# Performance work log

Hardware: AMD Instinct MI355X
Metric: run time of the kernel (lower is better)

Reference implementation:

```python
import jax, jax.numpy as jnp
import numpy as np

B, S, E, H = 2, 2048, 768, 12
DK = E // H


def setup_inputs() -> dict:
    key = jax.random.key(0)
    ks = jax.random.split(key, 8)
    scale = 1.0 / np.sqrt(E)
    return {
        "key": jax.random.normal(ks[0], (B, S, E), jnp.float32),
        "query": jax.random.normal(ks[1], (B, S, E), jnp.float32),
        "value": jax.random.normal(ks[2], (B, S, E), jnp.float32),
        "mask": jax.random.randint(ks[3], (1, 1, S, S), 0, 2, jnp.int32),
        # nn.Linear params (w_k used for q/k/v as in the source; w_o output proj)
        "Wk": jax.random.uniform(ks[4], (E, E), jnp.float32, -scale, scale),
        "bk": jax.random.uniform(ks[5], (E,), jnp.float32, -scale, scale),
        "Wo": jax.random.uniform(ks[6], (E, E), jnp.float32, -scale, scale),
        "bo": jax.random.uniform(ks[7], (E,), jnp.float32, -scale, scale),
    }


def reference(key, query, value, mask, Wk, bk, Wo, bo):
    # NOTE: source module (faithfully) projects q, k, v all with w_k.
    k = (key @ Wk.T + bk).reshape(B, S, H, DK).transpose(0, 2, 1, 3)    # [B,H,S,DK]
    q = (query @ Wk.T + bk).reshape(B, S, H, DK).transpose(0, 2, 1, 3)
    v = (value @ Wk.T + bk).reshape(B, S, H, DK).transpose(0, 2, 1, 3)
    # quirk: scores MULTIPLIED by sqrt(d_k) (source bug, preserved)
    scores = jnp.einsum("bhsd,bhtd->bhst", q, k) * jnp.sqrt(jnp.float32(DK))
    # quirk: masked positions set to 1e-6 (not -inf), BEFORE softmax
    scores = jnp.where(mask == 0, jnp.float32(1e-6), scores)
    # dropout=0.0 -> identity (applied pre-softmax in source)
    attn = jax.nn.softmax(scores, axis=-1)                               # [B,H,S,S]
    x = jnp.einsum("bhst,bhtd->bhsd", attn, v)                           # [B,H,S,DK]
    x = x.transpose(0, 2, 1, 3).reshape(B, S, E)
    return x @ Wo.T + bo
```

## Files before the change

kernel.cpp:

```cpp
#include <hip/hip_runtime.h>

#define BB 2
#define SS 2048
#define EE 768
#define HH 12
#define DKK 64

typedef _Float16 h16;
typedef _Float16 half8 __attribute__((ext_vector_type(8)));
typedef _Float16 h16x4 __attribute__((ext_vector_type(4)));
typedef __fp16 pk2 __attribute__((ext_vector_type(2)));
typedef float f32x4 __attribute__((ext_vector_type(4)));

#define K2F 11.5416173f

__device__ __forceinline__ void gl_lds16(const void* g, void* l) {
    __builtin_amdgcn_global_load_lds(
        (const __attribute__((address_space(1))) unsigned int*)g,
        (__attribute__((address_space(3))) unsigned int*)l, 16, 0, 0);
}

__global__ void cvtpack_k(const float* __restrict__ sK, const float* __restrict__ sQ,
                          const float* __restrict__ sV, const float* __restrict__ sWk,
                          const float* __restrict__ sWo,
                          h16* __restrict__ dK, h16* __restrict__ dQ, h16* __restrict__ dV,
                          h16* __restrict__ dWk, h16* __restrict__ dWo,
                          const int* __restrict__ mask, unsigned* __restrict__ mp) {
    if (blockIdx.x >= 5184) {
        int idx = (blockIdx.x - 5184) * 256 + threadIdx.x;
        int base = idx * 32;
        const int4* m4 = (const int4*)(mask + base);
        unsigned w = 0;
#pragma unroll
        for (int i = 0; i < 8; ++i) {
            int4 v = m4[i];
            if (v.x) w |= 1u << (i * 4 + 0);
            if (v.y) w |= 1u << (i * 4 + 1);
            if (v.z) w |= 1u << (i * 4 + 2);
            if (v.w) w |= 1u << (i * 4 + 3);
        }
        mp[idx] = w;
        return;
    }
    long g = (long)blockIdx.x * 256 + threadIdx.x;
    const float* src;
    h16* dst;
    long off;
    if (g < 393216)        { src = sK;  dst = dK;  off = g; }
    else if (g < 786432)   { src = sQ;  dst = dQ;  off = g - 393216; }
    else if (g < 1179648)  { src = sV;  dst = dV;  off = g - 786432; }
    else if (g < 1253376)  { src = sWk; dst = dWk; off = g - 1179648; }
    else                   { src = sWo; dst = dWo; off = g - 1253376; }
    const float* p = src + off * 8;
    float4 a = *(const float4*)p, b = *(const float4*)(p + 4);
    half8 h = {(h16)a.x, (h16)a.y, (h16)a.z, (h16)a.w,
               (h16)b.x, (h16)b.y, (h16)b.z, (h16)b.w};
    *(half8*)(dst + off * 8) = h;
}

__launch_bounds__(256)
__global__ void proj_gemm_k(const h16* __restrict__ keyh, const h16* __restrict__ qryh,
                            const h16* __restrict__ valh, const h16* __restrict__ Wkh,
                            const float* __restrict__ bk,
                            h16* __restrict__ kh, h16* __restrict__ qh, h16* __restrict__ vtp) {
    __shared__ h16 As[64 * 64];
    __shared__ h16 Bs[128 * 64];
    const int bid = blockIdx.x;
    const int idx = (bid & 7) * 144 + (bid >> 3);
    const int z = idx / 384;
    const int rem = idx % 384;
    const int m0 = (rem / 6) * 64, n0 = (rem % 6) * 128;
    const h16* src = (z == 0) ? keyh : ((z == 1) ? qryh : valh);
    const int tid = threadIdx.x, lane = tid & 63, wid = tid >> 6;
    const int l = lane & 15, gq = lane >> 4;
    f32x4 acc[4][2] = {};

    for (int k0 = 0; k0 < EE; k0 += 64) {
#pragma unroll
        for (int it = 0; it < 2; ++it) {
            int e = it * 256 + tid;
            int row = e >> 3, slot = e & 7;
            gl_lds16(src + (long)(m0 + row) * EE + k0 + ((slot ^ (row & 7)) << 3), As + e * 8);
        }
#pragma unroll
        for (int it = 0; it < 4; ++it) {
            int e = it * 256 + tid;
            int row = e >> 3, slot = e & 7;
            gl_lds16(Wkh + (long)(n0 + row) * EE + k0 + ((slot ^ (row & 7)) << 3), Bs + e * 8);
        }
        __syncthreads();
#pragma unroll
        for (int ks = 0; ks < 2; ++ks) {
            half8 a[4], b[2];
#pragma unroll
            for (int rf = 0; rf < 4; ++rf) {
                int row = rf * 16 + l;
                int g = (ks * 4 + gq) ^ (row & 7);
                a[rf] = *(const half8*)((const char*)As + row * 128 + (g << 4));
            }
#pragma unroll
            for (int cf = 0; cf < 2; ++cf) {
                int row = wid * 32 + cf * 16 + l;
                int g = (ks * 4 + gq) ^ (row & 7);
                b[cf] = *(const half8*)((const char*)Bs + row * 128 + (g << 4));
            }
            __builtin_amdgcn_s_setprio(1);
#pragma unroll
            for (int rf = 0; rf < 4; ++rf)
#pragma unroll
                for (int cf = 0; cf < 2; ++cf)
                    acc[rf][cf] = __builtin_amdgcn_mfma_f32_16x16x32_f16(a[rf], b[cf], acc[rf][cf], 0, 0, 0);
            __builtin_amdgcn_s_setprio(0);
        }
        __syncthreads();
    }
    if (z == 2) {
#pragma unroll
        for (int rf = 0; rf < 4; ++rf)
#pragma unroll
            for (int cf = 0; cf < 2; ++cf) {
                int n = n0 + wid * 32 + cf * 16 + l;
                float bias = bk[n];
                int h = n >> 6, d = n & 63;
                int mb = m0 + rf * 16 + gq * 4;
                int b = mb >> 11, s = mb & 2047;
                h16x4 pv = {(h16)(acc[rf][cf][0] + bias), (h16)(acc[rf][cf][1] + bias),
                            (h16)(acc[rf][cf][2] + bias), (h16)(acc[rf][cf][3] + bias)};
                *(h16x4*)(vtp + ((long)((b * HH + h) * 64 + d)) * SS + s) = pv;
            }
    } else {
        h16* dst = (z == 0) ? kh : qh;
        const float qs = (z == 1) ? K2F : 1.0f;
#pragma unroll
        for (int rf = 0; rf < 4; ++rf)
#pragma unroll
            for (int cf = 0; cf < 2; ++cf) {
                int n = n0 + wid * 32 + cf * 16 + l;
                float bias = bk[n];
                int h = n >> 6, d = n & 63;
#pragma unroll
                for (int j = 0; j < 4; ++j) {
                    int m = m0 + rf * 16 + gq * 4 + j;
                    int b = m >> 11, s = m & 2047;
                    dst[(((long)(b * HH + h) * SS + s) << 6) + d] = (h16)((acc[rf][cf][j] + bias) * qs);
                }
            }
    }
}

#define ATTN_TILE(KL, VL, KN, VN, T, KVN)                                          \
  {                                                                                \
    gl_lds16(kgl0 + (long)(KVN) * DKK, (KN) + stg0);                               \
    gl_lds16(kgl1 + (long)(KVN) * DKK, (KN) + stg1);                               \
    gl_lds16(vgl0 + (KVN), (VN) + stg0);                                           \
    gl_lds16(vgl1 + (KVN), (VN) + stg1);                                           \
    half8 ka[4], kb[4];                                                            \
    _Pragma("unroll")                                                              \
    for (int cf = 0; cf < 4; ++cf) {                                               \
      ka[cf] = *(const half8*)((const char*)(KL) + off0 + cf * 2048);              \
      kb[cf] = *(const half8*)((const char*)(KL) + off1 + cf * 2048);              \
    }                                                                              \
    f32x4 s[4];                                                                    \
    __builtin_amdgcn_s_setprio(1);                                                 \
    _Pragma("unroll")                                                              \
    for (int cf = 0; cf < 4; ++cf) {                                               \
      f32x4 z = {};                                                                \
      z = __builtin_amdgcn_mfma_f32_16x16x32_f16(ka[cf], qf0, z, 0, 0, 0);         \
      z = __builtin_amdgcn_mfma_f32_16x16x32_f16(kb[cf], qf1, z, 0, 0, 0);         \
      s[cf] = z;                                                                   \
    }                                                                              \
    __builtin_amdgcn_s_setprio(0);                                                 \
    unsigned long long mw = mrow[T];                                               \
    unsigned w0 = (unsigned)mw, w1 = (unsigned)(mw >> 32);                         \
    _Pragma("unroll")                                                              \
    for (int cf = 0; cf < 4; ++cf) {                                               \
      unsigned wcb = (cf & 2) ? w1 : w0;                                           \
      _Pragma("unroll")                                                            \
      for (int j = 0; j < 4; ++j) {                                                \
        unsigned sh = ((cf & 1) << 4) + g * 4 + j;                                 \
        s[cf][j] = ((wcb >> sh) & 1u) ? s[cf][j] : C2;                             \
      }                                                                            \
    }                                                                              \
    float pmax = fmaxf(fmaxf(s[0][0], s[0][1]), fmaxf(s[0][2], s[0][3]));          \
    _Pragma("unroll")                                                              \
    for (int cf = 1; cf < 4; ++cf)                                                 \
      pmax = fmaxf(pmax, fmaxf(fmaxf(s[cf][0], s[cf][1]), fmaxf(s[cf][2], s[cf][3]))); \
    if (!__all(pmax <= m2 + 11.0f)) {                                              \
      pmax = fmaxf(pmax, __shfl_xor(pmax, 16));                                    \
      pmax = fmaxf(pmax, __shfl_xor(pmax, 32));                                    \
      float mnew = fmaxf(m2, pmax);                                                \
      float alpha = __builtin_amdgcn_exp2f(m2 - mnew);                             \
      _Pragma("unroll")                                                            \
      for (int df = 0; df < 4; ++df)                                               \
        _Pragma("unroll")                                                          \
        for (int j = 0; j < 4; ++j) o[df][j] *= alpha;                             \
      lsum *= alpha;                                                               \
      m2 = mnew;                                                                   \
    }                                                                              \
    const float negm2 = -m2;                                                       \
    float rs = 0.f;                                                                \
    _Pragma("unroll")                                                              \
    for (int cf = 0; cf < 4; ++cf)                                                 \
      _Pragma("unroll")                                                            \
      for (int j = 0; j < 4; ++j) {                                                \
        float p = __builtin_amdgcn_exp2f(s[cf][j] + negm2);                        \
        s[cf][j] = p;                                                              \
        rs += p;                                                                   \
      }                                                                            \
    lsum += rs;                                                                    \
    _Pragma("unroll")                                                              \
    for (int cf = 0; cf < 4; ++cf) {                                               \
      union { pk2 h[2]; unsigned long long u; } pu;                                \
      pu.h[0] = __builtin_amdgcn_cvt_pkrtz(s[cf][0], s[cf][1]);                    \
      pu.h[1] = __builtin_amdgcn_cvt_pkrtz(s[cf][2], s[cf][3]);                    \
      *(unsigned long long*)(pbase + pst[cf]) = pu.u;                              \
    }                                                                              \
    _Pragma("unroll")                                                              \
    for (int ks = 0; ks < 2; ++ks) {                                               \
      half8 pf = *(const half8*)(pbase + (ks ? off1 : off0));                      \
      half8 vk[4];                                                                 \
      _Pragma("unroll")                                                            \
      for (int df = 0; df < 4; ++df)                                               \
        vk[df] = *(const half8*)((const char*)(VL) + (ks ? off1 : off0) + df * 2048); \
      __builtin_amdgcn_s_setprio(1);                                               \
      _Pragma("unroll")                                                            \
      for (int df = 0; df < 4; ++df)                                               \
        o[df] = __builtin_amdgcn_mfma_f32_16x16x32_f16(vk[df], pf, o[df], 0, 0, 0);\
      __builtin_amdgcn_s_setprio(0);                                               \
    }                                                                              \
    __syncthreads();                                                               \
  }

__launch_bounds__(256, 3)
__global__ void attn_k(const h16* __restrict__ qh, const h16* __restrict__ kh,
                       const h16* __restrict__ vt, const unsigned long long* __restrict__ mp,
                       h16* __restrict__ xh) {
    __shared__ h16 K0[4096], K1[4096], V0[4096], V1[4096];
    __shared__ char Ps[8192];
    const int tid = threadIdx.x;
    const int lane = tid & 63, wid = tid >> 6;
    const int l = lane & 15, g = lane >> 4;
    const int bid = blockIdx.x;
    const int idx = (bid & 7) * 96 + (bid >> 3);
    const int q0 = (idx & 31) * 64 + wid * 16;
    const int bh = idx >> 5;
    const long base = (long)bh * SS * DKK;
    char* pbase = Ps + wid * 2048;

    const int off0 = l * 128 + ((g ^ (l & 7)) << 4);
    const int off1 = l * 128 + (((4 + g) ^ (l & 7)) << 4);
    int pst[4];
#pragma unroll
    for (int cf = 0; cf < 4; ++cf)
        pst[cf] = l * 128 + (((2 * cf + (g >> 1)) ^ (l & 7)) << 4) + (g & 1) * 8;
    const int rr = lane >> 3, sg = (lane & 7) ^ (lane >> 3);
    const int stg0 = wid * 1024 + lane * 8, stg1 = wid * 1024 + 512 + lane * 8;
    const h16* kgl0 = kh + base + (long)(wid * 16 + rr) * DKK + sg * 8;
    const h16* kgl1 = kgl0 + 8 * DKK;
    const h16* vgl0 = vt + base + (long)(wid * 16 + rr) * SS + sg * 8;
    const h16* vgl1 = vgl0 + 8 * SS;

    half8 qf0, qf1;
    {
        const h16* qp = qh + base + (long)(q0 + l) * DKK + g * 8;
        qf0 = *(const half8*)qp;
        qf1 = *(const half8*)(qp + 32);
    }
    const unsigned long long* mrow = mp + (long)(q0 + l) * (SS / 64);

    f32x4 o[4] = {};
    float m2 = -INFINITY, lsum = 0.f;
    const float C2 = 1e-6f * 1.44269504f;

    gl_lds16(kgl0, K0 + stg0);
    gl_lds16(kgl1, K0 + stg1);
    gl_lds16(vgl0, V0 + stg0);
    gl_lds16(vgl1, V0 + stg1);
    __syncthreads();

    for (int it = 0; it < 16; ++it) {
        int t = 2 * it;
        ATTN_TILE(K0, V0, K1, V1, t, (t + 1) * 64)
        ATTN_TILE(K1, V1, K0, V0, t + 1, ((t + 2) & 31) * 64)
    }

    lsum += __shfl_xor(lsum, 16);
    lsum += __shfl_xor(lsum, 32);
    float inv = 1.0f / lsum;
    int b = bh / HH, h = bh % HH;
    h16* xp = xh + (long)(b * SS + q0 + l) * EE + h * 64 + g * 4;
#pragma unroll
    for (int df = 0; df < 4; ++df) {
        h16x4 v4 = {(h16)(o[df][0] * inv), (h16)(o[df][1] * inv),
                    (h16)(o[df][2] * inv), (h16)(o[df][3] * inv)};
        *(h16x4*)(xp + df * 16) = v4;
    }
}

__launch_bounds__(256)
__global__ void out_gemm_k(const h16* __restrict__ xh, const h16* __restrict__ Woh,
                           const float* __restrict__ bo, float* __restrict__ out) {
    __shared__ h16 As[64 * 64];
    __shared__ h16 Bs[64 * 64];
    const int bid = blockIdx.x;
    const int idx = (bid & 7) * 96 + (bid >> 3);
    const int m0 = (idx / 12) * 64, n0 = (idx % 12) * 64;
    const int tid = threadIdx.x, lane = tid & 63, wid = tid >> 6;
    const int l = lane & 15, gq = lane >> 4;
    const int wr = wid >> 1, wc = wid & 1;
    f32x4 acc[2][2] = {};

    for (int k0 = 0; k0 < EE; k0 += 64) {
#pragma unroll
        for (int it = 0; it < 2; ++it) {
            int e = it * 256 + tid;
            int row = e >> 3, slot = e & 7;
            int gsl = (slot ^ (row & 7)) << 3;
            gl_lds16(xh + (long)(m0 + row) * EE + k0 + gsl, As + e * 8);
            gl_lds16(Woh + (long)(n0 + row) * EE + k0 + gsl, Bs + e * 8);
        }
        __syncthreads();
#pragma unroll
        for (int ks = 0; ks < 2; ++ks) {
            half8 a[2], b[2];
#pragma unroll
            for (int rf = 0; rf < 2; ++rf) {
                int row = wr * 32 + rf * 16 + l;
                int g = (ks * 4 + gq) ^ (row & 7);
                a[rf] = *(const half8*)((const char*)As + row * 128 + (g << 4));
            }
#pragma unroll
            for (int cf = 0; cf < 2; ++cf) {
                int row = wc * 32 + cf * 16 + l;
                int g = (ks * 4 + gq) ^ (row & 7);
                b[cf] = *(const half8*)((const char*)Bs + row * 128 + (g << 4));
            }
            __builtin_amdgcn_s_setprio(1);
#pragma unroll
            for (int rf = 0; rf < 2; ++rf)
#pragma unroll
                for (int cf = 0; cf < 2; ++cf)
                    acc[rf][cf] = __builtin_amdgcn_mfma_f32_16x16x32_f16(a[rf], b[cf], acc[rf][cf], 0, 0, 0);
            __builtin_amdgcn_s_setprio(0);
        }
        __syncthreads();
    }
#pragma unroll
    for (int rf = 0; rf < 2; ++rf)
#pragma unroll
        for (int cf = 0; cf < 2; ++cf) {
            int n = n0 + wc * 32 + cf * 16 + l;
            float bias = bo[n];
#pragma unroll
            for (int j = 0; j < 4; ++j) {
                int m = m0 + wr * 32 + rf * 16 + gq * 4 + j;
                out[(long)m * EE + n] = acc[rf][cf][j] + bias;
            }
        }
}

extern "C" void kernel_launch(void* const* d_in, const int* in_sizes, int n_in,
                              void* d_out, int out_size, void* d_ws, size_t ws_size,
                              hipStream_t stream) {
    const float* key   = (const float*)d_in[0];
    const float* query = (const float*)d_in[1];
    const float* value = (const float*)d_in[2];
    const int*   mask  = (const int*)d_in[3];
    const float* Wk    = (const float*)d_in[4];
    const float* bk    = (const float*)d_in[5];
    const float* Wo    = (const float*)d_in[6];
    const float* bo    = (const float*)d_in[7];

    char* ws = (char*)d_ws;
    h16* keyh = (h16*)(ws + 0);
    h16* qryh = (h16*)(ws + 6291456);
    h16* valh = (h16*)(ws + 12582912);
    h16* qh   = (h16*)(ws + 18874368);
    h16* kh   = (h16*)(ws + 25165824);
    h16* vt   = (h16*)(ws + 31457280);
    h16* Wkh  = (h16*)(ws + 37748736);
    h16* Woh  = (h16*)(ws + 38928384);
    unsigned* mp = (unsigned*)(ws + 40108032);
    h16* xh = keyh;
    float* out = (float*)d_out;

    hipLaunchKernelGGL(cvtpack_k, dim3(5696), dim3(256), 0, stream,
                       key, query, value, Wk, Wo, keyh, qryh, valh, Wkh, Woh, mask, mp);
    hipLaunchKernelGGL(proj_gemm_k, dim3(1152), dim3(256), 0, stream,
                       keyh, qryh, valh, Wkh, bk, kh, qh, vt);
    hipLaunchKernelGGL(attn_k, dim3(SS / 64 * BB * HH), dim3(256), 0, stream,
                       qh, kh, vt, (const unsigned long long*)mp, xh);
    hipLaunchKernelGGL(out_gemm_k, dim3(768), dim3(256), 0, stream, xh, Woh, bo, out);
}
```

Baseline: 116.3 us.

## Split attention KV into halves with 32-row waves and add combine kernel

Each wave of the attention kernel now handles two 16-row query groups, so every K/V fragment read from LDS feeds twice as many MFMAs. The KV sequence is split into two halves, flash-decoding style, which keeps the grid at 768 blocks. A new combine kernel merges the two partial outputs using the saved max and sum values. The cost is an extra launch, extra global traffic for the fp16 partials, more registers per wave, and twice the LDS for P.

```diff
diff --git a/kernel.cpp b/kernel.cpp
--- a/kernel.cpp
+++ b/kernel.cpp
@@ -148,84 +148,104 @@
     }
 }
 
-#define ATTN_TILE(KL, VL, KN, VN, T, KVN)                                          \
+#define SMX_GROUP(S, MW, M2, LS, PB)                                               \
   {                                                                                \
-    gl_lds16(kgl0 + (long)(KVN) * DKK, (KN) + stg0);                               \
-    gl_lds16(kgl1 + (long)(KVN) * DKK, (KN) + stg1);                               \
-    gl_lds16(vgl0 + (KVN), (VN) + stg0);                                           \
-    gl_lds16(vgl1 + (KVN), (VN) + stg1);                                           \
+    unsigned long long mw = (MW);                                                  \
+    unsigned w0 = (unsigned)mw, w1 = (unsigned)(mw >> 32);                         \
+    _Pragma("unroll")                                                              \
+    for (int cf = 0; cf < 4; ++cf) {                                               \
+      unsigned wcb = (cf & 2) ? w1 : w0;                                           \
+      _Pragma("unroll")                                                            \
+      for (int j = 0; j < 4; ++j) {                                                \
+        unsigned sh = ((cf & 1) << 4) + g * 4 + j;                                 \
+        S[cf][j] = ((wcb >> sh) & 1u) ? S[cf][j] : C2;                             \
+      }                                                                            \
+    }                                                                              \
+    float pmax = fmaxf(fmaxf(S[0][0], S[0][1]), fmaxf(S[0][2], S[0][3]));          \
+    _Pragma("unroll")                                                              \
+    for (int cf = 1; cf < 4; ++cf)                                                 \
+      pmax = fmaxf(pmax, fmaxf(fmaxf(S[cf][0], S[cf][1]), fmaxf(S[cf][2], S[cf][3]))); \
+    if (!__all(pmax <= (M2) + 11.0f)) {                                            \
+      pmax = fmaxf(pmax, __shfl_xor(pmax, 16));                                    \
+      pmax = fmaxf(pmax, __shfl_xor(pmax, 32));                                    \
+      float mnew = fmaxf((M2), pmax);                                              \
+      float alpha = __builtin_amdgcn_exp2f((M2) - mnew);                           \
+      _Pragma("unroll")                                                            \
+      for (int df = 0; df < 4; ++df)                                               \
+        _Pragma("unroll")                                                          \
+        for (int j = 0; j < 4; ++j) o##PB[df][j] *= alpha;                         \
+      (LS) *= alpha;                                                               \
+      (M2) = mnew;                                                                 \
+    }                                                                              \
+    const float negm2 = -(M2);                                                     \
+    float rs = 0.f;                                                                \
+    _Pragma("unroll")                                                              \
+    for (int cf = 0; cf < 4; ++cf)                                                 \
+      _Pragma("unroll")                                                            \
+      for (int j = 0; j < 4; ++j) {                                                \
+        float p = __builtin_amdgcn_exp2f(S[cf][j] + negm2);                        \
+        S[cf][j] = p;                                                              \
+        rs += p;                                                                   \
+      }                                                                            \
+    (LS) += rs;                                                                    \
+    _Pragma("unroll")                                                              \
+    for (int cf = 0; cf < 4; ++cf) {                                               \
+      union { pk2 h[2]; unsigned long long u; } pu;                                \
+      pu.h[0] = __builtin_amdgcn_cvt_pkrtz(S[cf][0], S[cf][1]);                    \
+      pu.h[1] = __builtin_amdgcn_cvt_pkrtz(S[cf][2], S[cf][3]);                    \
+      *(unsigned long long*)(pb##PB + pst[cf]) = pu.u;                             \
+    }                                                                              \
+  }
+
+#define ATTN_TILE(KL, VL, KN, VN, T)                                               \
+  {                                                                                \
+    long nko = (long)((((T) + 1) & 15)) * (64 * DKK);                              \
+    int nvo = (((T) + 1) & 15) * 64;                                               \
+    gl_lds16(kgl0 + nko, (KN) + stg0);                                             \
+    gl_lds16(kgl1 + nko, (KN) + stg1);                                             \
+    gl_lds16(vgl0 + nvo, (VN) + stg0);                                             \
+    gl_lds16(vgl1 + nvo, (VN) + stg1);                                             \
     half8 ka[4], kb[4];                                                            \
     _Pragma("unroll")                                                              \
     for (int cf = 0; cf < 4; ++cf) {                                               \
       ka[cf] = *(const half8*)((const char*)(KL) + off0 + cf * 2048);              \
       kb[cf] = *(const half8*)((const char*)(KL) + off1 + cf * 2048);              \
     }                                                                              \
-    f32x4 s[4];                                                                    \
+    f32x4 sA[4], sB[4];                                                            \
     __builtin_amdgcn_s_setprio(1);                                                 \
     _Pragma("unroll")                                                              \
     for (int cf = 0; cf < 4; ++cf) {                                               \
       f32x4 z = {};                                                                \
-      z = __builtin_amdgcn_mfma_f32_16x16x32_f16(ka[cf], qf0, z, 0, 0, 0);         \
-      z = __builtin_amdgcn_mfma_f32_16x16x32_f16(kb[cf], qf1, z, 0, 0, 0);         \
-      s[cf] = z;                                                                   \
+      z = __builtin_amdgcn_mfma_f32_16x16x32_f16(ka[cf], qfA0, z, 0, 0, 0);        \
+      z = __builtin_amdgcn_mfma_f32_16x16x32_f16(kb[cf], qfA1, z, 0, 0, 0);        \
+      sA[cf] = z;                                                                  \
+    }                                                                              \
+    _Pragma("unroll")                                                              \
+    for (int cf = 0; cf < 4; ++cf) {                                               \
+      f32x4 z = {};                                                                \
+      z = __builtin_amdgcn_mfma_f32_16x16x32_f16(ka[cf], qfB0, z, 0, 0, 0);        \
+      z = __builtin_amdgcn_mfma_f32_16x16x32_f16(kb[cf], qfB1, z, 0, 0, 0);        \
+      sB[cf] = z;                                                                  \
     }                                                                              \
     __builtin_amdgcn_s_setprio(0);                                                 \
-    unsigned long long mw = mrow[T];                                               \
-    unsigned w0 = (unsigned)mw, w1 = (unsigned)(mw >> 32);                         \
-    _Pragma("unroll")                                                              \
-    for (int cf = 0; cf < 4; ++cf) {                                               \
-      unsigned wcb = (cf & 2) ? w1 : w0;                                           \
-      _Pragma("unroll")                                                            \
-      for (int j = 0; j < 4; ++j) {                                                \
-        unsigned sh = ((cf & 1) << 4) + g * 4 + j;                                 \
-        s[cf][j] = ((wcb >> sh) & 1u) ? s[cf][j] : C2;                             \
-      }                                                                            \
-    }                                                                              \
-    float pmax = fmaxf(fmaxf(s[0][0], s[0][1]), fmaxf(s[0][2], s[0][3]));          \
-    _Pragma("unroll")                                                              \
-    for (int cf = 1; cf < 4; ++cf)                                                 \
-      pmax = fmaxf(pmax, fmaxf(fmaxf(s[cf][0], s[cf][1]), fmaxf(s[cf][2], s[cf][3]))); \
-    if (!__all(pmax <= m2 + 11.0f)) {                                              \
-      pmax = fmaxf(pmax, __shfl_xor(pmax, 16));                                    \
-      pmax = fmaxf(pmax, __shfl_xor(pmax, 32));                                    \
-      float mnew = fmaxf(m2, pmax);                                                \
-      float alpha = __builtin_amdgcn_exp2f(m2 - mnew);                             \
+    SMX_GROUP(sA, mrA[T], m2A, lsA, A)                                             \
+    SMX_GROUP(sB, mrB[T], m2B, lsB, B)                                             \
+    _Pragma("unroll")                                                              \
+    for (int ks = 0; ks < 2; ++ks) {                                               \
+      int fo = ks ? off1 : off0;                                                   \
+      half8 vk[4];                                                                 \
       _Pragma("unroll")                                                            \
       for (int df = 0; df < 4; ++df)                                               \
-        _Pragma("unroll")                                                          \
-        for (int j = 0; j < 4; ++j) o[df][j] *= alpha;                             \
-      lsum *= alpha;                                                               \
-      m2 = mnew;                                                                   \
-    }                                                                              \
-    const float negm2 = -m2;                                                       \
-    float rs = 0.f;                                                                \
-    _Pragma("unroll")                                                              \
-    for (int cf = 0; cf < 4; ++cf)                                                 \
-      _Pragma("unroll")                                                            \
-      for (int j = 0; j < 4; ++j) {                                                \
-        float p = __builtin_amdgcn_exp2f(s[cf][j] + negm2);                        \
-        s[cf][j] = p;                                                              \
-        rs += p;                                                                   \
-      }                                                                            \
-    lsum += rs;                                                                    \
-    _Pragma("unroll")                                                              \
-    for (int cf = 0; cf < 4; ++cf) {                                               \
-      union { pk2 h[2]; unsigned long long u; } pu;                                \
-      pu.h[0] = __builtin_amdgcn_cvt_pkrtz(s[cf][0], s[cf][1]);                    \
-      pu.h[1] = __builtin_amdgcn_cvt_pkrtz(s[cf][2], s[cf][3]);                    \
-      *(unsigned long long*)(pbase + pst[cf]) = pu.u;                              \
-    }                                                                              \
-    _Pragma("unroll")                                                              \
-    for (int ks = 0; ks < 2; ++ks) {                                               \
-      half8 pf = *(const half8*)(pbase + (ks ? off1 : off0));                      \
-      half8 vk[4];                                                                 \
+        vk[df] = *(const half8*)((const char*)(VL) + fo + df * 2048);              \
+      half8 pfA = *(const half8*)(pbA + fo);                                       \
+      half8 pfB = *(const half8*)(pbB + fo);                                       \
+      __builtin_amdgcn_s_setprio(1);                                               \
       _Pragma("unroll")                                                            \
       for (int df = 0; df < 4; ++df)                                               \
-        vk[df] = *(const half8*)((const char*)(VL) + (ks ? off1 : off0) + df * 2048); \
-      __builtin_amdgcn_s_setprio(1);                                               \
+        oA[df] = __builtin_amdgcn_mfma_f32_16x16x32_f16(vk[df], pfA, oA[df], 0, 0, 0); \
       _Pragma("unroll")                                                            \
       for (int df = 0; df < 4; ++df)                                               \
-        o[df] = __builtin_amdgcn_mfma_f32_16x16x32_f16(vk[df], pf, o[df], 0, 0, 0);\
+        oB[df] = __builtin_amdgcn_mfma_f32_16x16x32_f16(vk[df], pfB, oB[df], 0, 0, 0); \
       __builtin_amdgcn_s_setprio(0);                                               \
     }                                                                              \
     __syncthreads();                                                               \
@@ -234,18 +254,21 @@
 __launch_bounds__(256, 3)
 __global__ void attn_k(const h16* __restrict__ qh, const h16* __restrict__ kh,
                        const h16* __restrict__ vt, const unsigned long long* __restrict__ mp,
-                       h16* __restrict__ xh) {
+                       h16* __restrict__ pO, float* __restrict__ pML) {
     __shared__ h16 K0[4096], K1[4096], V0[4096], V1[4096];
-    __shared__ char Ps[8192];
+    __shared__ char Ps[16384];
     const int tid = threadIdx.x;
     const int lane = tid & 63, wid = tid >> 6;
     const int l = lane & 15, g = lane >> 4;
     const int bid = blockIdx.x;
     const int idx = (bid & 7) * 96 + (bid >> 3);
-    const int q0 = (idx & 31) * 64 + wid * 16;
     const int bh = idx >> 5;
+    const int rem = idx & 31;
+    const int qb = rem >> 1, kvh = rem & 1;
+    const int q0w = qb * 128 + wid * 32;
     const long base = (long)bh * SS * DKK;
-    char* pbase = Ps + wid * 2048;
+    char* pbA = Ps + wid * 4096;
+    char* pbB = pbA + 2048;
 
     const int off0 = l * 128 + ((g ^ (l & 7)) << 4);
     const int off1 = l * 128 + (((4 + g) ^ (l & 7)) << 4);
@@ -255,21 +278,25 @@
         pst[cf] = l * 128 + (((2 * cf + (g >> 1)) ^ (l & 7)) << 4) + (g & 1) * 8;
     const int rr = lane >> 3, sg = (lane & 7) ^ (lane >> 3);
     const int stg0 = wid * 1024 + lane * 8, stg1 = wid * 1024 + 512 + lane * 8;
-    const h16* kgl0 = kh + base + (long)(wid * 16 + rr) * DKK + sg * 8;
+    const int kvbase = kvh * 1024;
+    const h16* kgl0 = kh + base + (long)(kvbase + wid * 16 + rr) * DKK + sg * 8;
     const h16* kgl1 = kgl0 + 8 * DKK;
-    const h16* vgl0 = vt + base + (long)(wid * 16 + rr) * SS + sg * 8;
+    const h16* vgl0 = vt + base + (long)(wid * 16 + rr) * SS + kvbase + sg * 8;
     const h16* vgl1 = vgl0 + 8 * SS;
 
-    half8 qf0, qf1;
+    half8 qfA0, qfA1, qfB0, qfB1;
     {
-        const h16* qp = qh + base + (long)(q0 + l) * DKK + g * 8;
-        qf0 = *(const half8*)qp;
-        qf1 = *(const half8*)(qp + 32);
-    }
-    const unsigned long long* mrow = mp + (long)(q0 + l) * (SS / 64);
-
-    f32x4 o[4] = {};
-    float m2 = -INFINITY, lsum = 0.f;
+        const h16* qp = qh + base + (long)(q0w + l) * DKK + g * 8;
+        qfA0 = *(const half8*)qp;
+        qfA1 = *(const half8*)(qp + 32);
+        qfB0 = *(const half8*)(qp + 16 * DKK);
+        qfB1 = *(const half8*)(qp + 16 * DKK + 32);
+    }
+    const unsigned long long* mrA = mp + (long)(q0w + l) * (SS / 64) + kvh * 16;
+    const unsigned long long* mrB = mrA + 16 * (SS / 64);
+
+    f32x4 oA[4] = {}, oB[4] = {};
+    float m2A = -INFINITY, lsA = 0.f, m2B = -INFINITY, lsB = 0.f;
     const float C2 = 1e-6f * 1.44269504f;
 
     gl_lds16(kgl0, K0 + stg0);
@@ -278,23 +305,55 @@
     gl_lds16(vgl1, V0 + stg1);
     __syncthreads();
 
-    for (int it = 0; it < 16; ++it) {
+    for (int it = 0; it < 8; ++it) {
         int t = 2 * it;
-        ATTN_TILE(K0, V0, K1, V1, t, (t + 1) * 64)
-        ATTN_TILE(K1, V1, K0, V0, t + 1, ((t + 2) & 31) * 64)
-    }
-
-    lsum += __shfl_xor(lsum, 16);
-    lsum += __shfl_xor(lsum, 32);
-    float inv = 1.0f / lsum;
+        ATTN_TILE(K0, V0, K1, V1, t)
+        ATTN_TILE(K1, V1, K0, V0, t + 1)
+    }
+
+    lsA += __shfl_xor(lsA, 16);
+    lsA += __shfl_xor(lsA, 32);
+    lsB += __shfl_xor(lsB, 16);
+    lsB += __shfl_xor(lsB, 32);
+    long prow = ((long)(bh * 2 + kvh) * 2048 + q0w + l);
+    h16* pa = pO + (prow << 6) + g * 4;
+    h16* pb = pO + ((prow + 16) << 6) + g * 4;
+#pragma unroll
+    for (int df = 0; df < 4; ++df) {
+        h16x4 vA = {(h16)oA[df][0], (h16)oA[df][1], (h16)oA[df][2], (h16)oA[df][3]};
+        h16x4 vB = {(h16)oB[df][0], (h16)oB[df][1], (h16)oB[df][2], (h16)oB[df][3]};
+        *(h16x4*)(pa + df * 16) = vA;
+        *(h16x4*)(pb + df * 16) = vB;
+    }
+    if (g == 0) {
+        float2* mlp = (float2*)(pML + prow * 2);
+        *mlp = make_float2(m2A, lsA);
+        *(float2*)(pML + (prow + 16) * 2) = make_float2(m2B, lsB);
+    }
+}
+
+__global__ void combine_k(const h16* __restrict__ pO, const float* __restrict__ pML,
+                          h16* __restrict__ xh) {
+    int idx = blockIdx.x * 256 + threadIdx.x;
+    int d8 = idx & 7;
+    int q = (idx >> 3) & 2047;
+    int bh = idx >> 14;
+    long r0 = (long)(bh * 2) * 2048 + q, r1 = r0 + 2048;
+    float2 ml0 = *(const float2*)(pML + r0 * 2);
+    float2 ml1 = *(const float2*)(pML + r1 * 2);
+    float ms = fmaxf(ml0.x, ml1.x);
+    float w0 = __builtin_amdgcn_exp2f(ml0.x - ms);
+    float w1 = __builtin_amdgcn_exp2f(ml1.x - ms);
+    float inv = 1.0f / (ml0.y * w0 + ml1.y * w1);
+    float s0 = w0 * inv, s1 = w1 * inv;
+    half8 o0 = *(const half8*)(pO + (r0 << 6) + d8 * 8);
+    half8 o1 = *(const half8*)(pO + (r1 << 6) + d8 * 8);
     int b = bh / HH, h = bh % HH;
-    h16* xp = xh + (long)(b * SS + q0 + l) * EE + h * 64 + g * 4;
-#pragma unroll
-    for (int df = 0; df < 4; ++df) {
-        h16x4 v4 = {(h16)(o[df][0] * inv), (h16)(o[df][1] * inv),
-                    (h16)(o[df][2] * inv), (h16)(o[df][3] * inv)};
-        *(h16x4*)(xp + df * 16) = v4;
-    }
+    half8 r;
+#pragma unroll
+    for (int i = 0; i < 8; ++i)
+        r[i] = (h16)((float)o0[i] * s0 + (float)o1[i] * s1);
+    *(half8*)(xh + (long)(b * SS + q) * EE + h * 64 + d8 * 8) = r;
 }
 
 __launch_bounds__(256)
@@ -381,14 +440,17 @@
     h16* Wkh  = (h16*)(ws + 37748736);
     h16* Woh  = (h16*)(ws + 38928384);
     unsigned* mp = (unsigned*)(ws + 40108032);
-    h16* xh = keyh;
+    h16*  pO  = (h16*)(ws + 0);
+    float* pML = (float*)(ws + 12582912);
+    h16*  xh  = (h16*)(ws + 18874368);
     float* out = (float*)d_out;
 
     hipLaunchKernelGGL(cvtpack_k, dim3(5696), dim3(256), 0, stream,
                        key, query, value, Wk, Wo, keyh, qryh, valh, Wkh, Woh, mask, mp);
     hipLaunchKernelGGL(proj_gemm_k, dim3(1152), dim3(256), 0, stream,
                        keyh, qryh, valh, Wkh, bk, kh, qh, vt);
-    hipLaunchKernelGGL(attn_k, dim3(SS / 64 * BB * HH), dim3(256), 0, stream,
-                       qh, kh, vt, (const unsigned long long*)mp, xh);
+    hipLaunchKernelGGL(attn_k, dim3(768), dim3(256), 0, stream,
+                       qh, kh, vt, (const unsigned long long*)mp, pO, pML);
+    hipLaunchKernelGGL(combine_k, dim3(1536), dim3(256), 0, stream, pO, pML, xh);
     hipLaunchKernelGGL(out_gemm_k, dim3(768), dim3(256), 0, stream, xh, Woh, bo, out);
 }
```

New measurement: 115.9 us. Within noise of the previous version (-0.3%).
